# Kernel tuning notes

Measured on AMD Instinct MI355X. Metric: run time of the kernel, lower is better.

## Reference

```python
import jax, jax.numpy as jnp
import numpy as np

N_NODES = 500_000   # number of mesh nodes
N_ELEM = 1_000_000  # number of linear triangular elements
N_PTS = 8_388_608   # number of evaluation points
DIM = 2             # 2D problem: nodal_values has one field per spatial dim


def setup_inputs() -> dict:
    key = jax.random.key(0)
    k1, k2, k3, k4 = jax.random.split(key, 4)
    # 1-based node IDs as in the original (forward subtracts 1).
    connectivity = jax.random.randint(k1, (N_ELEM, 3), 1, N_NODES + 1, dtype=jnp.int32)
    cell_id = jax.random.randint(k2, (N_PTS,), 0, N_ELEM, dtype=jnp.int32)
    nodal_values = jax.random.normal(k3, (DIM, N_NODES), dtype=jnp.float32)
    shape_functions = jax.random.uniform(k4, (N_PTS, 3), dtype=jnp.float32)
    return {
        "nodal_values": nodal_values,
        "shape_functions": shape_functions,
        "connectivity": connectivity,
        "cell_id": cell_id,
    }


def reference(nodal_values, shape_functions, connectivity, cell_id):
    # connectivity[cell_id] - 1 : [N_PTS, 3] zero-based node IDs per point
    ids = connectivity[cell_id] - 1
    # Gather nodal values for the 3 nodes of each point's element: [DIM, N_PTS, 3]
    vals = nodal_values[:, ids]
    # u = N1*v1 + N2*v2 + N3*v3 per point, per spatial dim -> [DIM, N_PTS]
    u = jnp.einsum('nk,dnk->dn', shape_functions, vals)
    return u
```

## Files before the change

kernel.cpp:

```cpp
#include <hip/hip_runtime.h>
#include <hip/hip_bf16.h>

#define N_NODES 500000
#define N_ELEM  1000000
#define N_PTS   8388608

typedef float f32x4 __attribute__((ext_vector_type(4)));
typedef int   i32x4 __attribute__((ext_vector_type(4)));
typedef unsigned int u32x2 __attribute__((ext_vector_type(2)));
typedef unsigned int u32x8 __attribute__((ext_vector_type(8)));

__device__ __forceinline__ u32x2 encode6(const float v[6]) {
    float m = fabsf(v[0]);
#pragma unroll
    for (int k = 1; k < 6; ++k) m = fmaxf(m, fabsf(v[k]));
    unsigned mb = __float_as_uint(m);
    int e = (int)(mb >> 23) - 127 + 1;
    e = min(7, max(-8, e));
    const float inv = __uint_as_float((unsigned)(9 - e + 127) << 23);
    int q[6];
#pragma unroll
    for (int k = 0; k < 6; ++k) {
        int qi = __float2int_rn(v[k] * inv);
        q[k] = min(511, max(-512, qi));
    }
    const unsigned eb = (unsigned)(e + 8);
    u32x2 row;
    row.x = (q[0] & 1023u) | ((q[1] & 1023u) << 10) | ((q[2] & 1023u) << 20)
          | ((eb & 3u) << 30);
    row.y = (q[3] & 1023u) | ((q[4] & 1023u) << 10) | ((q[5] & 1023u) << 20)
          | ((eb >> 2) << 30);
    return row;
}

__global__ __launch_bounds__(256) void pack_kernel(
    const float* __restrict__ nodal,
    const i32x4* __restrict__ conn4,
    u32x8* __restrict__ packed8)
{
    const int t = blockIdx.x * blockDim.x + threadIdx.x;
    if (t >= N_ELEM / 4) return;

    const i32x4 c0 = __builtin_nontemporal_load(&conn4[3 * t + 0]);
    const i32x4 c1 = __builtin_nontemporal_load(&conn4[3 * t + 1]);
    const i32x4 c2 = __builtin_nontemporal_load(&conn4[3 * t + 2]);
    const int idx[12] = {c0.x - 1, c0.y - 1, c0.z - 1, c0.w - 1,
                         c1.x - 1, c1.y - 1, c1.z - 1, c1.w - 1,
                         c2.x - 1, c2.y - 1, c2.z - 1, c2.w - 1};

    u32x8 outrow;
#pragma unroll
    for (int el = 0; el < 4; ++el) {
        const int n0 = idx[3 * el + 0];
        const int n1 = idx[3 * el + 1];
        const int n2 = idx[3 * el + 2];
        float v[6];
        v[0] = nodal[n0];
        v[1] = nodal[n1];
        v[2] = nodal[n2];
        v[3] = nodal[N_NODES + n0];
        v[4] = nodal[N_NODES + n1];
        v[5] = nodal[N_NODES + n2];
        const u32x2 r = encode6(v);
        outrow[2 * el + 0] = r.x;
        outrow[2 * el + 1] = r.y;
    }
    __builtin_nontemporal_store(outrow, &packed8[t]);
}

__global__ __launch_bounds__(256) void interp2d_packed_kernel(
    const u32x2* __restrict__ packed,
    const f32x4* __restrict__ sf4,
    const i32x4* __restrict__ cell4,
    float* __restrict__ out)
{
    const int t = blockIdx.x * blockDim.x + threadIdx.x;
    if (t >= N_PTS / 8) return;

    const i32x4 ca = __builtin_nontemporal_load(&cell4[2 * t + 0]);
    const i32x4 cb = __builtin_nontemporal_load(&cell4[2 * t + 1]);
    const int cids[8] = {ca.x, ca.y, ca.z, ca.w, cb.x, cb.y, cb.z, cb.w};

    u32x2 row[8];
#pragma unroll
    for (int j = 0; j < 8; ++j) row[j] = packed[cids[j]];

    f32x4 s[6];
#pragma unroll
    for (int k = 0; k < 6; ++k)
        s[k] = __builtin_nontemporal_load(&sf4[6 * t + k]);

    float w[24];
#pragma unroll
    for (int k = 0; k < 6; ++k) {
        w[4 * k + 0] = s[k].x;
        w[4 * k + 1] = s[k].y;
        w[4 * k + 2] = s[k].z;
        w[4 * k + 3] = s[k].w;
    }

    float u0[8], u1[8];
#pragma unroll
    for (int j = 0; j < 8; ++j) {
        const unsigned lo = row[j].x;
        const unsigned hi = row[j].y;
        const unsigned eb = ((lo >> 30) & 3u) | (((hi >> 30) & 3u) << 2);
        const float scale = __uint_as_float((eb + 110u) << 23);
        const float f0 = (float)(((int)(lo << 22)) >> 22);
        const float f1 = (float)(((int)(lo << 12)) >> 22);
        const float f2 = (float)(((int)(lo <<  2)) >> 22);
        const float f3 = (float)(((int)(hi << 22)) >> 22);
        const float f4 = (float)(((int)(hi << 12)) >> 22);
        const float f5 = (float)(((int)(hi <<  2)) >> 22);
        const float w0 = w[3 * j + 0];
        const float w1 = w[3 * j + 1];
        const float w2 = w[3 * j + 2];
        u0[j] = (w0 * f0 + w1 * f1 + w2 * f2) * scale;
        u1[j] = (w0 * f3 + w1 * f4 + w2 * f5) * scale;
    }

    f32x4 o0a = {u0[0], u0[1], u0[2], u0[3]};
    f32x4 o0b = {u0[4], u0[5], u0[6], u0[7]};
    f32x4 o1a = {u1[0], u1[1], u1[2], u1[3]};
    f32x4 o1b = {u1[4], u1[5], u1[6], u1[7]};
    f32x4* out0 = reinterpret_cast<f32x4*>(out);
    f32x4* out1 = reinterpret_cast<f32x4*>(out + N_PTS);
    __builtin_nontemporal_store(o0a, &out0[2 * t + 0]);
    __builtin_nontemporal_store(o0b, &out0[2 * t + 1]);
    __builtin_nontemporal_store(o1a, &out1[2 * t + 0]);
    __builtin_nontemporal_store(o1b, &out1[2 * t + 1]);
}

__global__ __launch_bounds__(256) void interp2d_direct_kernel(
    const float* __restrict__ nodal,
    const f32x4* __restrict__ sf4,
    const int* __restrict__ conn,
    const i32x4* __restrict__ cell4,
    float* __restrict__ out)
{
    const int t = blockIdx.x * blockDim.x + threadIdx.x;
    if (t >= N_PTS / 4) return;

    const i32x4 cid = cell4[t];
    const f32x4 s0 = sf4[3 * t + 0];
    const f32x4 s1 = sf4[3 * t + 1];
    const f32x4 s2 = sf4[3 * t + 2];

    const float w[4][3] = {
        {s0.x, s0.y, s0.z},
        {s0.w, s1.x, s1.y},
        {s1.z, s1.w, s2.x},
        {s2.y, s2.z, s2.w},
    };
    const int cids[4] = {cid.x, cid.y, cid.z, cid.w};

    float u0[4], u1[4];
#pragma unroll
    for (int j = 0; j < 4; ++j) {
        const int* cr = conn + 3 * (long)cids[j];
        const int i0 = cr[0] - 1;
        const int i1 = cr[1] - 1;
        const int i2 = cr[2] - 1;
        u0[j] = w[j][0] * nodal[i0] + w[j][1] * nodal[i1] + w[j][2] * nodal[i2];
        u1[j] = w[j][0] * nodal[N_NODES + i0] + w[j][1] * nodal[N_NODES + i1]
              + w[j][2] * nodal[N_NODES + i2];
    }

    f32x4 o0 = {u0[0], u0[1], u0[2], u0[3]};
    f32x4 o1 = {u1[0], u1[1], u1[2], u1[3]};
    reinterpret_cast<f32x4*>(out)[t] = o0;
    reinterpret_cast<f32x4*>(out + N_PTS)[t] = o1;
}

extern "C" void kernel_launch(void* const* d_in, const int* in_sizes, int n_in,
                              void* d_out, int out_size, void* d_ws, size_t ws_size,
                              hipStream_t stream) {
    const float* nodal = (const float*)d_in[0];
    const float* sf    = (const float*)d_in[1];
    const int*   conn  = (const int*)d_in[2];
    const int*   cell  = (const int*)d_in[3];
    float* out = (float*)d_out;

    const int block = 256;
    const size_t packed_bytes = (size_t)N_ELEM * 8;

    if (ws_size >= packed_bytes) {
        const int e4 = N_ELEM / 4;
        pack_kernel<<<(e4 + block - 1) / block, block, 0, stream>>>(
            nodal,
            reinterpret_cast<const i32x4*>(conn),
            (u32x8*)d_ws);

        const int p8 = N_PTS / 8;
        interp2d_packed_kernel<<<p8 / block, block, 0, stream>>>(
            (const u32x2*)d_ws,
            reinterpret_cast<const f32x4*>(sf),
            reinterpret_cast<const i32x4*>(cell),
            out);
    } else {
        const int n_threads = N_PTS / 4;
        interp2d_direct_kernel<<<(n_threads + block - 1) / block, block, 0, stream>>>(
            nodal,
            reinterpret_cast<const f32x4*>(sf),
            conn,
            reinterpret_cast<const i32x4*>(cell),
            out);
    }
}
```

Before: 169.1 us.

## Split packed element table per dimension and run one interp pass per dim

The packed element table is rebuilt as two 4-byte-per-element tables, one per spatial dimension, each holding three 9-bit quantized values and a 4-bit exponent. The interpolation kernel then runs twice, once per table, so each random-gather working set is half as large and more likely to stay cache-resident. In exchange, cell_id and the shape functions are streamed twice. Quantization precision also drops from 10 to 9 bits, which could push errors closer to the tolerance.

```diff
diff --git a/kernel.cpp b/kernel.cpp
--- a/kernel.cpp
+++ b/kernel.cpp
@@ -7,36 +7,25 @@
 
 typedef float f32x4 __attribute__((ext_vector_type(4)));
 typedef int   i32x4 __attribute__((ext_vector_type(4)));
-typedef unsigned int u32x2 __attribute__((ext_vector_type(2)));
-typedef unsigned int u32x8 __attribute__((ext_vector_type(8)));
+typedef unsigned int u32x4 __attribute__((ext_vector_type(4)));
 
-__device__ __forceinline__ u32x2 encode6(const float v[6]) {
-    float m = fabsf(v[0]);
-#pragma unroll
-    for (int k = 1; k < 6; ++k) m = fmaxf(m, fabsf(v[k]));
-    unsigned mb = __float_as_uint(m);
-    int e = (int)(mb >> 23) - 127 + 1;
+__device__ __forceinline__ unsigned encode3(float v0, float v1, float v2) {
+    const float m = fmaxf(fmaxf(fabsf(v0), fabsf(v1)), fabsf(v2));
+    int e = (int)(__float_as_uint(m) >> 23) - 126;
     e = min(7, max(-8, e));
-    const float inv = __uint_as_float((unsigned)(9 - e + 127) << 23);
-    int q[6];
-#pragma unroll
-    for (int k = 0; k < 6; ++k) {
-        int qi = __float2int_rn(v[k] * inv);
-        q[k] = min(511, max(-512, qi));
-    }
+    const float inv = __uint_as_float((unsigned)(135 - e) << 23);
+    const int q0 = min(255, max(-256, __float2int_rn(v0 * inv)));
+    const int q1 = min(255, max(-256, __float2int_rn(v1 * inv)));
+    const int q2 = min(255, max(-256, __float2int_rn(v2 * inv)));
     const unsigned eb = (unsigned)(e + 8);
-    u32x2 row;
-    row.x = (q[0] & 1023u) | ((q[1] & 1023u) << 10) | ((q[2] & 1023u) << 20)
-          | ((eb & 3u) << 30);
-    row.y = (q[3] & 1023u) | ((q[4] & 1023u) << 10) | ((q[5] & 1023u) << 20)
-          | ((eb >> 2) << 30);
-    return row;
+    return (q0 & 511u) | ((q1 & 511u) << 9) | ((q2 & 511u) << 18) | (eb << 27);
 }
 
 __global__ __launch_bounds__(256) void pack_kernel(
     const float* __restrict__ nodal,
     const i32x4* __restrict__ conn4,
-    u32x8* __restrict__ packed8)
+    u32x4* __restrict__ table0_4,
+    u32x4* __restrict__ table1_4)
 {
     const int t = blockIdx.x * blockDim.x + threadIdx.x;
     if (t >= N_ELEM / 4) return;
@@ -48,31 +37,25 @@
                          c1.x - 1, c1.y - 1, c1.z - 1, c1.w - 1,
                          c2.x - 1, c2.y - 1, c2.z - 1, c2.w - 1};
 
-    u32x8 outrow;
+    u32x4 r0, r1;
 #pragma unroll
     for (int el = 0; el < 4; ++el) {
         const int n0 = idx[3 * el + 0];
         const int n1 = idx[3 * el + 1];
         const int n2 = idx[3 * el + 2];
-        float v[6];
-        v[0] = nodal[n0];
-        v[1] = nodal[n1];
-        v[2] = nodal[n2];
-        v[3] = nodal[N_NODES + n0];
-        v[4] = nodal[N_NODES + n1];
-        v[5] = nodal[N_NODES + n2];
-        const u32x2 r = encode6(v);
-        outrow[2 * el + 0] = r.x;
-        outrow[2 * el + 1] = r.y;
+        r0[el] = encode3(nodal[n0], nodal[n1], nodal[n2]);
+        r1[el] = encode3(nodal[N_NODES + n0], nodal[N_NODES + n1],
+                         nodal[N_NODES + n2]);
     }
-    __builtin_nontemporal_store(outrow, &packed8[t]);
+    table0_4[t] = r0;
+    table1_4[t] = r1;
 }
 
-__global__ __launch_bounds__(256) void interp2d_packed_kernel(
-    const u32x2* __restrict__ packed,
+__global__ __launch_bounds__(256) void interp_dim_kernel(
+    const unsigned* __restrict__ table,
     const f32x4* __restrict__ sf4,
     const i32x4* __restrict__ cell4,
-    float* __restrict__ out)
+    float* __restrict__ outdim)
 {
     const int t = blockIdx.x * blockDim.x + threadIdx.x;
     if (t >= N_PTS / 8) return;
@@ -81,9 +64,9 @@
     const i32x4 cb = __builtin_nontemporal_load(&cell4[2 * t + 1]);
     const int cids[8] = {ca.x, ca.y, ca.z, ca.w, cb.x, cb.y, cb.z, cb.w};
 
-    u32x2 row[8];
+    unsigned row[8];
 #pragma unroll
-    for (int j = 0; j < 8; ++j) row[j] = packed[cids[j]];
+    for (int j = 0; j < 8; ++j) row[j] = table[cids[j]];
 
     f32x4 s[6];
 #pragma unroll
@@ -99,36 +82,23 @@
         w[4 * k + 3] = s[k].w;
     }
 
-    float u0[8], u1[8];
+    float u[8];
 #pragma unroll
     for (int j = 0; j < 8; ++j) {
-        const unsigned lo = row[j].x;
-        const unsigned hi = row[j].y;
-        const unsigned eb = ((lo >> 30) & 3u) | (((hi >> 30) & 3u) << 2);
-        const float scale = __uint_as_float((eb + 110u) << 23);
-        const float f0 = (float)(((int)(lo << 22)) >> 22);
-        const float f1 = (float)(((int)(lo << 12)) >> 22);
-        const float f2 = (float)(((int)(lo <<  2)) >> 22);
-        const float f3 = (float)(((int)(hi << 22)) >> 22);
-        const float f4 = (float)(((int)(hi << 12)) >> 22);
-        const float f5 = (float)(((int)(hi <<  2)) >> 22);
-        const float w0 = w[3 * j + 0];
-        const float w1 = w[3 * j + 1];
-        const float w2 = w[3 * j + 2];
-        u0[j] = (w0 * f0 + w1 * f1 + w2 * f2) * scale;
-        u1[j] = (w0 * f3 + w1 * f4 + w2 * f5) * scale;
+        const unsigned r = row[j];
+        const float scale = __uint_as_float((((r >> 27) & 15u) + 111u) << 23);
+        const float f0 = (float)(((int)(r << 23)) >> 23);
+        const float f1 = (float)(((int)(r << 14)) >> 23);
+        const float f2 = (float)(((int)(r <<  5)) >> 23);
+        u[j] = (w[3 * j + 0] * f0 + w[3 * j + 1] * f1 + w[3 * j + 2] * f2)
+             * scale;
     }
 
-    f32x4 o0a = {u0[0], u0[1], u0[2], u0[3]};
-    f32x4 o0b = {u0[4], u0[5], u0[6], u0[7]};
-    f32x4 o1a = {u1[0], u1[1], u1[2], u1[3]};
-    f32x4 o1b = {u1[4], u1[5], u1[6], u1[7]};
-    f32x4* out0 = reinterpret_cast<f32x4*>(out);
-    f32x4* out1 = reinterpret_cast<f32x4*>(out + N_PTS);
-    __builtin_nontemporal_store(o0a, &out0[2 * t + 0]);
-    __builtin_nontemporal_store(o0b, &out0[2 * t + 1]);
-    __builtin_nontemporal_store(o1a, &out1[2 * t + 0]);
-    __builtin_nontemporal_store(o1b, &out1[2 * t + 1]);
+    f32x4 oa = {u[0], u[1], u[2], u[3]};
+    f32x4 ob = {u[4], u[5], u[6], u[7]};
+    f32x4* o = reinterpret_cast<f32x4*>(outdim);
+    __builtin_nontemporal_store(oa, &o[2 * t + 0]);
+    __builtin_nontemporal_store(ob, &o[2 * t + 1]);
 }
 
 __global__ __launch_bounds__(256) void interp2d_direct_kernel(
@@ -185,18 +155,27 @@
     const size_t packed_bytes = (size_t)N_ELEM * 8;
 
     if (ws_size >= packed_bytes) {
+        unsigned* table0 = (unsigned*)d_ws;
+        unsigned* table1 = table0 + N_ELEM;
+
         const int e4 = N_ELEM / 4;
         pack_kernel<<<(e4 + block - 1) / block, block, 0, stream>>>(
             nodal,
             reinterpret_cast<const i32x4*>(conn),
-            (u32x8*)d_ws);
+            reinterpret_cast<u32x4*>(table0),
+            reinterpret_cast<u32x4*>(table1));
 
         const int p8 = N_PTS / 8;
-        interp2d_packed_kernel<<<p8 / block, block, 0, stream>>>(
-            (const u32x2*)d_ws,
+        interp_dim_kernel<<<p8 / block, block, 0, stream>>>(
+            table0,
             reinterpret_cast<const f32x4*>(sf),
             reinterpret_cast<const i32x4*>(cell),
             out);
+        interp_dim_kernel<<<p8 / block, block, 0, stream>>>(
+            table1,
+            reinterpret_cast<const f32x4*>(sf),
+            reinterpret_cast<const i32x4*>(cell),
+            out + N_PTS);
     } else {
         const int n_threads = N_PTS / 4;
         interp2d_direct_kernel<<<(n_threads + block - 1) / block, block, 0, stream>>>(
```

Result: slower. 214.1 us (+26.6%).
